# Kernel optimization log

Hardware: AMD Instinct MI355X
Metric: run time of the kernel (lower is better)

## Reference

```python
import jax, jax.numpy as jnp
import numpy as np

MARGIN = 1.0


def setup_inputs() -> dict:
    key = jax.random.key(0)
    k1, k2, k3 = jax.random.split(key, 3)
    n, d = 8192, 128
    feat1 = jax.random.normal(k1, (n, d), dtype=jnp.float32)
    feat2 = jax.random.normal(k2, (n, d), dtype=jnp.float32)
    # similarity labels in {+1, -1}, as expected by HingeEmbeddingLoss
    simi = (2 * jax.random.randint(k3, (n, n), 0, 2) - 1).astype(jnp.int32)
    return {"feat1": feat1, "feat2": feat2, "simi": simi}


def reference(feat1, feat2, simi):
    # logits[i,j] = -||feat1_i - feat2_j||^2, computed without the O(n*m*d) expand
    sq1 = jnp.sum(feat1 * feat1, axis=-1, keepdims=True)          # [n, 1]
    sq2 = jnp.sum(feat2 * feat2, axis=-1)                          # [m]
    cross = jnp.einsum('nd,md->nm', feat1, feat2)                  # [n, m]
    logits = -(sq1 + sq2[None, :] - 2.0 * cross)                   # [n, m]
    probs = jax.nn.softmax(logits, axis=1)                         # [n, m]
    # HingeEmbeddingLoss: x if y==1 else max(0, margin - x); mean reduction
    loss = jnp.where(simi == 1, probs, jnp.maximum(0.0, MARGIN - probs))
    return jnp.mean(loss)
```

## Files before the change

### kernel.cpp

```cpp
#include <hip/hip_runtime.h>
#include <hip/hip_bf16.h>
#include <stdint.h>

#define N 8192
#define D 128
#define NCHUNK 16
#define CHUNK (N / NCHUNK)
#define RT 128
#define CT 64
#define NTILES (CHUNK / CT)
#define NBLK (N / RT * NCHUNK)

typedef short bf16x8 __attribute__((ext_vector_type(8)));
typedef float f32x4 __attribute__((ext_vector_type(4)));
typedef unsigned int uint32;

#define OFF_ACC   0u
#define OFF_SQ2   1024u
#define OFF_BCNT  (OFF_SQ2 + N * 4u)
#define OFF_M     (OFF_BCNT + NBLK * 4u)
#define OFF_L     (OFF_M + NCHUNK * N * 4u)
#define OFF_S     (OFF_L + NCHUNK * N * 4u)
#define OFF_F1    (OFF_S + NCHUNK * N * 4u)
#define OFF_F2    (OFF_F1 + N * D * 2u)

__global__ __launch_bounds__(256)
void prep_kernel(const float* __restrict__ f1, const float* __restrict__ f2,
                 unsigned short* __restrict__ f1b, unsigned short* __restrict__ f2b,
                 float* __restrict__ sq2) {
    const int w    = blockIdx.x * 4 + (threadIdx.x >> 6);
    const int lane = threadIdx.x & 63;
    for (int row = w; row < N; row += 1024) {
        float a0 = f1[row * D + lane];
        float a1 = f1[row * D + 64 + lane];
        float b0 = f2[row * D + lane];
        float b1 = f2[row * D + 64 + lane];
        __hip_bfloat16 t;
        t = __float2bfloat16(a0); f1b[row * D + lane]      = *(unsigned short*)&t;
        t = __float2bfloat16(a1); f1b[row * D + 64 + lane] = *(unsigned short*)&t;
        t = __float2bfloat16(b0); f2b[row * D + lane]      = *(unsigned short*)&t;
        t = __float2bfloat16(b1); f2b[row * D + 64 + lane] = *(unsigned short*)&t;
        float ss = b0 * b0 + b1 * b1;
        #pragma unroll
        for (int off = 32; off > 0; off >>= 1) ss += __shfl_xor(ss, off);
        if (lane == 0) sq2[row] = ss;
    }
}

__global__ __launch_bounds__(256)
void main_kernel(const unsigned short* __restrict__ f1b,
                 const unsigned short* __restrict__ f2b,
                 const float* __restrict__ sq2,
                 const int* __restrict__ simi,
                 float* __restrict__ pm, float* __restrict__ pl, float* __restrict__ ps,
                 uint32* __restrict__ blockcnt) {
    __shared__ unsigned short ldsB[CT * D];
    __shared__ uint32 cred[4];

    const int tid  = threadIdx.x;
    const int wave = tid >> 6;
    const int lane = tid & 63;
    const int lo   = lane & 15;
    const int hi   = lane >> 4;

    const int rowtile = blockIdx.x;
    const int chunk   = blockIdx.y;
    const int rbase   = rowtile * RT + wave * 32;
    const int cbase0  = chunk * CHUNK;

    bf16x8 afrag[2][4];
    #pragma unroll
    for (int a = 0; a < 2; a++) {
        const unsigned short* ap = f1b + (size_t)(rbase + a * 16 + lo) * D + hi * 8;
        #pragma unroll
        for (int kk = 0; kk < 4; kk++)
            afrag[a][kk] = *reinterpret_cast<const bf16x8*>(ap + kk * 32);
    }

    const int sq_ = (tid >> 4);
    const int sg_ = tid & 15;
    const unsigned short* stg_p[4];
    #pragma unroll
    for (int it = 0; it < 4; it++) {
        int q = it * 16 + sq_;
        int c = 4 * (q & 15) + (q >> 4);
        stg_p[it] = f2b + (size_t)(cbase0 + c) * D + sg_ * 8;
    }
    unsigned short* lds_p[4];
    #pragma unroll
    for (int it = 0; it < 4; it++) {
        int q = it * 16 + sq_;
        lds_p[it] = ldsB + q * D + ((sg_ ^ (q & 15)) * 8);
    }

    const int* simi_p = simi + (size_t)(rbase + hi * 4) * N + cbase0 + 4 * lo;
    const float* sqv_p = sq2 + cbase0 + 4 * lo;

    float m[2][4], l[2][4], s[2][4];
    #pragma unroll
    for (int a = 0; a < 2; a++)
        #pragma unroll
        for (int r = 0; r < 4; r++) { m[a][r] = -1e30f; l[a][r] = 0.f; s[a][r] = 0.f; }
    uint32 cnt = 0;

    int4 mkv[2][4];
    uint4 vstg[4];
    f32x4 sqv;
    #pragma unroll
    for (int a = 0; a < 2; a++)
        #pragma unroll
        for (int r = 0; r < 4; r++)
            mkv[a][r] = *reinterpret_cast<const int4*>(simi_p + (size_t)(a * 16 + r) * N);
    #pragma unroll
    for (int it = 0; it < 4; it++)
        vstg[it] = *reinterpret_cast<const uint4*>(stg_p[it]);
    sqv = *reinterpret_cast<const f32x4*>(sqv_p);

    for (int t = 0; t < NTILES; t++) {
        __syncthreads();
        #pragma unroll
        for (int it = 0; it < 4; it++)
            *reinterpret_cast<uint4*>(lds_p[it]) = vstg[it];
        __syncthreads();

        uint32 mb[2][4];
        #pragma unroll
        for (int a = 0; a < 2; a++)
            #pragma unroll
            for (int r = 0; r < 4; r++) {
                int4 v = mkv[a][r];
                uint32 nib = (uint32)(v.x == 1) | ((uint32)(v.y == 1) << 1) |
                             ((uint32)(v.z == 1) << 2) | ((uint32)(v.w == 1) << 3);
                mb[a][r] = nib;
                cnt += 4u - __popc(nib);
            }
        f32x4 sqv_t = sqv;

        if (t + 1 < NTILES) {
            const int* sp = simi_p + CT;
            #pragma unroll
            for (int a = 0; a < 2; a++)
                #pragma unroll
                for (int r = 0; r < 4; r++)
                    mkv[a][r] = *reinterpret_cast<const int4*>(sp + (size_t)(a * 16 + r) * N);
            #pragma unroll
            for (int it = 0; it < 4; it++)
                vstg[it] = *reinterpret_cast<const uint4*>(stg_p[it] + (size_t)(t + 1) * CT * D);
            sqv = *reinterpret_cast<const f32x4*>(sqv_p + (t + 1) * CT);
            simi_p = sp;
        }

        f32x4 acc[2][4];
        #pragma unroll
        for (int cf = 0; cf < 4; cf++) {
            acc[0][cf] = (f32x4){0.f, 0.f, 0.f, 0.f};
            acc[1][cf] = (f32x4){0.f, 0.f, 0.f, 0.f};
            const int brow = cf * 16 + lo;
            #pragma unroll
            for (int kk = 0; kk < 4; kk++) {
                int g = kk * 4 + hi;
                bf16x8 b = *reinterpret_cast<const bf16x8*>(
                    ldsB + brow * D + ((g ^ (brow & 15)) * 8));
                acc[0][cf] = __builtin_amdgcn_mfma_f32_16x16x32_bf16(afrag[0][kk], b, acc[0][cf], 0, 0, 0);
                acc[1][cf] = __builtin_amdgcn_mfma_f32_16x16x32_bf16(afrag[1][kk], b, acc[1][cf], 0, 0, 0);
            }
        }

        #pragma unroll
        for (int a = 0; a < 2; a++)
            #pragma unroll
            for (int r = 0; r < 4; r++) {
                float lg[4];
                #pragma unroll
                for (int cf = 0; cf < 4; cf++)
                    lg[cf] = 2.0f * acc[a][cf][r] - sqv_t[cf];
                float tm = fmaxf(fmaxf(lg[0], lg[1]), fmaxf(lg[2], lg[3]));
                float mn = fmaxf(m[a][r], tm);
                float al = __expf(m[a][r] - mn);
                m[a][r] = mn;
                float p[4];
                #pragma unroll
                for (int cf = 0; cf < 4; cf++) p[cf] = __expf(lg[cf] - mn);
                l[a][r] = l[a][r] * al + ((p[0] + p[1]) + (p[2] + p[3]));
                float sm = 0.f;
                #pragma unroll
                for (int cf = 0; cf < 4; cf++)
                    sm += ((mb[a][r] >> cf) & 1u) ? p[cf] : 0.f;
                s[a][r] = s[a][r] * al + sm;
            }
    }

    #pragma unroll
    for (int a = 0; a < 2; a++)
        #pragma unroll
        for (int r = 0; r < 4; r++) {
            float M = m[a][r];
            #pragma unroll
            for (int off = 1; off < 16; off <<= 1)
                M = fmaxf(M, __shfl_xor(M, off));
            float sc = __expf(m[a][r] - M);
            float L = l[a][r] * sc, S = s[a][r] * sc;
            #pragma unroll
            for (int off = 1; off < 16; off <<= 1) {
                L += __shfl_xor(L, off);
                S += __shfl_xor(S, off);
            }
            if (lo == 0) {
                int row = rbase + a * 16 + hi * 4 + r;
                int idx = chunk * N + row;
                pm[idx] = M; pl[idx] = L; ps[idx] = S;
            }
        }

    #pragma unroll
    for (int off = 1; off < 64; off <<= 1) cnt += __shfl_xor(cnt, off);
    if (lane == 0) cred[wave] = cnt;
    __syncthreads();
    if (tid == 0)
        blockcnt[blockIdx.y * 64 + blockIdx.x] = cred[0] + cred[1] + cred[2] + cred[3];
}

__global__ void merge_kernel(const float* __restrict__ pm, const float* __restrict__ pl,
                             const float* __restrict__ ps, const uint32* __restrict__ blockcnt,
                             float* __restrict__ s_acc, uint32* __restrict__ neg_acc) {
    const int row = blockIdx.x * 256 + threadIdx.x;
    float M = -1e30f;
    #pragma unroll
    for (int k = 0; k < NCHUNK; k++) M = fmaxf(M, pm[k * N + row]);
    float L = 0.f, S = 0.f;
    #pragma unroll
    for (int k = 0; k < NCHUNK; k++) {
        float e = __expf(pm[k * N + row] - M);
        L += pl[k * N + row] * e;
        S += ps[k * N + row] * e;
    }
    float r = S / L;
    uint32 pc = (threadIdx.x < 32) ? blockcnt[blockIdx.x * 32 + threadIdx.x] : 0u;
    #pragma unroll
    for (int off = 32; off > 0; off >>= 1) {
        r  += __shfl_xor(r, off);
        pc += __shfl_xor(pc, off);
    }
    __shared__ float red[4];
    __shared__ uint32 redp[4];
    int lane = threadIdx.x & 63, w = threadIdx.x >> 6;
    if (lane == 0) { red[w] = r; redp[w] = pc; }
    __syncthreads();
    if (threadIdx.x == 0) {
        atomicAdd(s_acc, red[0] + red[1] + red[2] + red[3]);
        atomicAdd(neg_acc, redp[0] + redp[1] + redp[2] + redp[3]);
    }
}

__global__ void final_kernel(const float* __restrict__ s_acc, const uint32* __restrict__ neg_acc,
                             float* __restrict__ out) {
    double S = (double)s_acc[0];
    double C = (double)neg_acc[0];
    double n = (double)N;
    out[0] = (float)((2.0 * S + C - n) / (n * n));
}

extern "C" void kernel_launch(void* const* d_in, const int* in_sizes, int n_in,
                              void* d_out, int out_size, void* d_ws, size_t ws_size,
                              hipStream_t stream) {
    const float* f1   = (const float*)d_in[0];
    const float* f2   = (const float*)d_in[1];
    const int*   simi = (const int*)d_in[2];
    float* out = (float*)d_out;
    char* ws = (char*)d_ws;

    float*  acc_s    = (float*)(ws + OFF_ACC);
    uint32* acc_n    = (uint32*)(ws + OFF_ACC + 4);
    float*  sq2      = (float*)(ws + OFF_SQ2);
    uint32* blockcnt = (uint32*)(ws + OFF_BCNT);
    float*  pm       = (float*)(ws + OFF_M);
    float*  pl       = (float*)(ws + OFF_L);
    float*  ps       = (float*)(ws + OFF_S);
    unsigned short* f1b = (unsigned short*)(ws + OFF_F1);
    unsigned short* f2b = (unsigned short*)(ws + OFF_F2);

    hipMemsetAsync(ws + OFF_ACC, 0, 64, stream);
    prep_kernel<<<256, 256, 0, stream>>>(f1, f2, f1b, f2b, sq2);
    main_kernel<<<dim3(N / RT, NCHUNK), 256, 0, stream>>>(f1b, f2b, sq2, simi,
                                                          pm, pl, ps, blockcnt);
    merge_kernel<<<N / 256, 256, 0, stream>>>(pm, pl, ps, blockcnt, acc_s, acc_n);
    final_kernel<<<1, 1, 0, stream>>>(acc_s, acc_n, out);
}
```

Measured before the change: 427.1 us.

## Halve row tile and stream simi mask via global_load_lds double buffer

Cuts rows per block from 128 to 64, so each wave handles one 16-row MFMA fragment and the grid doubles. The simi label tiles are now loaded straight into a double-buffered LDS area with global_load_lds instead of into registers, which lowers register pressure and should raise occupancy and memory parallelism on this bandwidth-bound int32 mask stream. The cost is that each f2 tile is staged to LDS twice as often in total, and LDS use grows by 32 KB per block. The blockcnt indexing in the merge step is updated to match.

Result: no change. 426.2 us (-0.2%).

```diff
diff --git a/kernel.cpp b/kernel.cpp
--- a/kernel.cpp
+++ b/kernel.cpp
@@ -6,7 +6,7 @@
 #define D 128
 #define NCHUNK 16
 #define CHUNK (N / NCHUNK)
-#define RT 128
+#define RT 64
 #define CT 64
 #define NTILES (CHUNK / CT)
 #define NBLK (N / RT * NCHUNK)
@@ -23,6 +23,11 @@
 #define OFF_S     (OFF_L + NCHUNK * N * 4u)
 #define OFF_F1    (OFF_S + NCHUNK * N * 4u)
 #define OFF_F2    (OFF_F1 + N * D * 2u)
+
+#define GLLDS16(gp, lp)                                                        \
+    __builtin_amdgcn_global_load_lds(                                          \
+        (const __attribute__((address_space(1))) uint32*)(gp),                 \
+        (__attribute__((address_space(3))) uint32*)(lp), 16, 0, 0)
 
 __global__ __launch_bounds__(256)
 void prep_kernel(const float* __restrict__ f1, const float* __restrict__ f2,
@@ -55,6 +60,7 @@
                  float* __restrict__ pm, float* __restrict__ pl, float* __restrict__ ps,
                  uint32* __restrict__ blockcnt) {
     __shared__ unsigned short ldsB[CT * D];
+    __shared__ uint32 maskMem[2 * 4 * 4 * 256];
     __shared__ uint32 cred[4];
 
     const int tid  = threadIdx.x;
@@ -65,56 +71,48 @@
 
     const int rowtile = blockIdx.x;
     const int chunk   = blockIdx.y;
-    const int rbase   = rowtile * RT + wave * 32;
+    const int rbase   = rowtile * RT + wave * 16;
     const int cbase0  = chunk * CHUNK;
 
-    bf16x8 afrag[2][4];
-    #pragma unroll
-    for (int a = 0; a < 2; a++) {
-        const unsigned short* ap = f1b + (size_t)(rbase + a * 16 + lo) * D + hi * 8;
+    bf16x8 afrag[4];
+    {
+        const unsigned short* ap = f1b + (size_t)(rbase + lo) * D + hi * 8;
         #pragma unroll
         for (int kk = 0; kk < 4; kk++)
-            afrag[a][kk] = *reinterpret_cast<const bf16x8*>(ap + kk * 32);
+            afrag[kk] = *reinterpret_cast<const bf16x8*>(ap + kk * 32);
     }
 
     const int sq_ = (tid >> 4);
     const int sg_ = tid & 15;
     const unsigned short* stg_p[4];
+    unsigned short* lds_p[4];
     #pragma unroll
     for (int it = 0; it < 4; it++) {
         int q = it * 16 + sq_;
         int c = 4 * (q & 15) + (q >> 4);
         stg_p[it] = f2b + (size_t)(cbase0 + c) * D + sg_ * 8;
-    }
-    unsigned short* lds_p[4];
-    #pragma unroll
-    for (int it = 0; it < 4; it++) {
-        int q = it * 16 + sq_;
         lds_p[it] = ldsB + q * D + ((sg_ ^ (q & 15)) * 8);
     }
 
     const int* simi_p = simi + (size_t)(rbase + hi * 4) * N + cbase0 + 4 * lo;
     const float* sqv_p = sq2 + cbase0 + 4 * lo;
-
-    float m[2][4], l[2][4], s[2][4];
-    #pragma unroll
-    for (int a = 0; a < 2; a++)
-        #pragma unroll
-        for (int r = 0; r < 4; r++) { m[a][r] = -1e30f; l[a][r] = 0.f; s[a][r] = 0.f; }
+    uint32* mbase[2];
+    mbase[0] = maskMem + wave * 4 * 256;
+    mbase[1] = maskMem + (4 + wave) * 4 * 256;
+
+    float m[4], l[4], s[4];
+    #pragma unroll
+    for (int r = 0; r < 4; r++) { m[r] = -1e30f; l[r] = 0.f; s[r] = 0.f; }
     uint32 cnt = 0;
 
-    int4 mkv[2][4];
+    #pragma unroll
+    for (int r = 0; r < 4; r++)
+        GLLDS16(simi_p + (size_t)r * N, mbase[0] + r * 256);
     uint4 vstg[4];
-    f32x4 sqv;
-    #pragma unroll
-    for (int a = 0; a < 2; a++)
-        #pragma unroll
-        for (int r = 0; r < 4; r++)
-            mkv[a][r] = *reinterpret_cast<const int4*>(simi_p + (size_t)(a * 16 + r) * N);
     #pragma unroll
     for (int it = 0; it < 4; it++)
         vstg[it] = *reinterpret_cast<const uint4*>(stg_p[it]);
-    sqv = *reinterpret_cast<const f32x4*>(sqv_p);
+    f32x4 sqv = *reinterpret_cast<const f32x4*>(sqv_p);
 
     for (int t = 0; t < NTILES; t++) {
         __syncthreads();
@@ -123,26 +121,23 @@
             *reinterpret_cast<uint4*>(lds_p[it]) = vstg[it];
         __syncthreads();
 
-        uint32 mb[2][4];
-        #pragma unroll
-        for (int a = 0; a < 2; a++)
-            #pragma unroll
-            for (int r = 0; r < 4; r++) {
-                int4 v = mkv[a][r];
-                uint32 nib = (uint32)(v.x == 1) | ((uint32)(v.y == 1) << 1) |
-                             ((uint32)(v.z == 1) << 2) | ((uint32)(v.w == 1) << 3);
-                mb[a][r] = nib;
-                cnt += 4u - __popc(nib);
-            }
+        const uint32* mk = mbase[t & 1];
+        uint32 mb[4];
+        #pragma unroll
+        for (int r = 0; r < 4; r++) {
+            int4 v = *reinterpret_cast<const int4*>(mk + r * 256 + lane * 4);
+            uint32 nib = (uint32)(v.x == 1) | ((uint32)(v.y == 1) << 1) |
+                         ((uint32)(v.z == 1) << 2) | ((uint32)(v.w == 1) << 3);
+            mb[r] = nib;
+            cnt += 4u - __popc(nib);
+        }
         f32x4 sqv_t = sqv;
 
         if (t + 1 < NTILES) {
             const int* sp = simi_p + CT;
             #pragma unroll
-            for (int a = 0; a < 2; a++)
-                #pragma unroll
-                for (int r = 0; r < 4; r++)
-                    mkv[a][r] = *reinterpret_cast<const int4*>(sp + (size_t)(a * 16 + r) * N);
+            for (int r = 0; r < 4; r++)
+                GLLDS16(sp + (size_t)r * N, mbase[(t + 1) & 1] + r * 256);
             #pragma unroll
             for (int it = 0; it < 4; it++)
                 vstg[it] = *reinterpret_cast<const uint4*>(stg_p[it] + (size_t)(t + 1) * CT * D);
@@ -150,74 +145,68 @@
             simi_p = sp;
         }
 
-        f32x4 acc[2][4];
+        f32x4 acc[4];
         #pragma unroll
         for (int cf = 0; cf < 4; cf++) {
-            acc[0][cf] = (f32x4){0.f, 0.f, 0.f, 0.f};
-            acc[1][cf] = (f32x4){0.f, 0.f, 0.f, 0.f};
+            acc[cf] = (f32x4){0.f, 0.f, 0.f, 0.f};
             const int brow = cf * 16 + lo;
             #pragma unroll
             for (int kk = 0; kk < 4; kk++) {
                 int g = kk * 4 + hi;
                 bf16x8 b = *reinterpret_cast<const bf16x8*>(
                     ldsB + brow * D + ((g ^ (brow & 15)) * 8));
-                acc[0][cf] = __builtin_amdgcn_mfma_f32_16x16x32_bf16(afrag[0][kk], b, acc[0][cf], 0, 0, 0);
-                acc[1][cf] = __builtin_amdgcn_mfma_f32_16x16x32_bf16(afrag[1][kk], b, acc[1][cf], 0, 0, 0);
+                acc[cf] = __builtin_amdgcn_mfma_f32_16x16x32_bf16(afrag[kk], b, acc[cf], 0, 0, 0);
             }
         }
 
         #pragma unroll
-        for (int a = 0; a < 2; a++)
-            #pragma unroll
-            for (int r = 0; r < 4; r++) {
-                float lg[4];
-                #pragma unroll
-                for (int cf = 0; cf < 4; cf++)
-                    lg[cf] = 2.0f * acc[a][cf][r] - sqv_t[cf];
-                float tm = fmaxf(fmaxf(lg[0], lg[1]), fmaxf(lg[2], lg[3]));
-                float mn = fmaxf(m[a][r], tm);
-                float al = __expf(m[a][r] - mn);
-                m[a][r] = mn;
-                float p[4];
-                #pragma unroll
-                for (int cf = 0; cf < 4; cf++) p[cf] = __expf(lg[cf] - mn);
-                l[a][r] = l[a][r] * al + ((p[0] + p[1]) + (p[2] + p[3]));
-                float sm = 0.f;
-                #pragma unroll
-                for (int cf = 0; cf < 4; cf++)
-                    sm += ((mb[a][r] >> cf) & 1u) ? p[cf] : 0.f;
-                s[a][r] = s[a][r] * al + sm;
-            }
-    }
-
-    #pragma unroll
-    for (int a = 0; a < 2; a++)
-        #pragma unroll
         for (int r = 0; r < 4; r++) {
-            float M = m[a][r];
-            #pragma unroll
-            for (int off = 1; off < 16; off <<= 1)
-                M = fmaxf(M, __shfl_xor(M, off));
-            float sc = __expf(m[a][r] - M);
-            float L = l[a][r] * sc, S = s[a][r] * sc;
-            #pragma unroll
-            for (int off = 1; off < 16; off <<= 1) {
-                L += __shfl_xor(L, off);
-                S += __shfl_xor(S, off);
-            }
-            if (lo == 0) {
-                int row = rbase + a * 16 + hi * 4 + r;
-                int idx = chunk * N + row;
-                pm[idx] = M; pl[idx] = L; ps[idx] = S;
-            }
-        }
+            float lg[4];
+            #pragma unroll
+            for (int cf = 0; cf < 4; cf++)
+                lg[cf] = 2.0f * acc[cf][r] - sqv_t[cf];
+            float tm = fmaxf(fmaxf(lg[0], lg[1]), fmaxf(lg[2], lg[3]));
+            float mn = fmaxf(m[r], tm);
+            float al = __expf(m[r] - mn);
+            m[r] = mn;
+            float p[4];
+            #pragma unroll
+            for (int cf = 0; cf < 4; cf++) p[cf] = __expf(lg[cf] - mn);
+            l[r] = l[r] * al + ((p[0] + p[1]) + (p[2] + p[3]));
+            float sm = 0.f;
+            #pragma unroll
+            for (int cf = 0; cf < 4; cf++)
+                sm += ((mb[r] >> cf) & 1u) ? p[cf] : 0.f;
+            s[r] = s[r] * al + sm;
+        }
+    }
+
+    #pragma unroll
+    for (int r = 0; r < 4; r++) {
+        float M = m[r];
+        #pragma unroll
+        for (int off = 1; off < 16; off <<= 1)
+            M = fmaxf(M, __shfl_xor(M, off));
+        float sc = __expf(m[r] - M);
+        float L = l[r] * sc, S = s[r] * sc;
+        #pragma unroll
+        for (int off = 1; off < 16; off <<= 1) {
+            L += __shfl_xor(L, off);
+            S += __shfl_xor(S, off);
+        }
+        if (lo == 0) {
+            int row = rbase + hi * 4 + r;
+            int idx = chunk * N + row;
+            pm[idx] = M; pl[idx] = L; ps[idx] = S;
+        }
+    }
 
     #pragma unroll
     for (int off = 1; off < 64; off <<= 1) cnt += __shfl_xor(cnt, off);
     if (lane == 0) cred[wave] = cnt;
     __syncthreads();
     if (tid == 0)
-        blockcnt[blockIdx.y * 64 + blockIdx.x] = cred[0] + cred[1] + cred[2] + cred[3];
+        blockcnt[blockIdx.y * 128 + blockIdx.x] = cred[0] + cred[1] + cred[2] + cred[3];
 }
 
 __global__ void merge_kernel(const float* __restrict__ pm, const float* __restrict__ pl,
@@ -235,7 +224,7 @@
         S += ps[k * N + row] * e;
     }
     float r = S / L;
-    uint32 pc = (threadIdx.x < 32) ? blockcnt[blockIdx.x * 32 + threadIdx.x] : 0u;
+    uint32 pc = (threadIdx.x < 64) ? blockcnt[blockIdx.x * 64 + threadIdx.x] : 0u;
     #pragma unroll
     for (int off = 32; off > 0; off >>= 1) {
         r  += __shfl_xor(r, off);
```
